# Kernel optimization log

Measured on AMD Instinct MI355X. Metric: run time of the kernel, lower is better.

## Reference

```python
import jax, jax.numpy as jnp
import numpy as np

NEG_INF = -1e30

def setup_inputs() -> dict:
    key = jax.random.key(0)
    ks = jax.random.split(key, 8)
    N, E = 4096, 16384
    Fn, Fe, Dn, De = 128, 64, 128, 64
    # xavier_uniform bound = sqrt(6/(fan_in+fan_out)); for 1-D params torch treats shape as (1, len)
    bn = np.sqrt(6.0 / (Fn + Dn))
    be = np.sqrt(6.0 / (Fe + De))
    return {
        "node_features": jax.random.normal(ks[0], (N, Fn), dtype=jnp.float32),
        "edge_features": jax.random.normal(ks[1], (E, Fe), dtype=jnp.float32),
        "adjacency_matrix": jax.random.randint(ks[2], (N, N), 0, 2, dtype=jnp.int32),
        "edge_adjacency_matrix": jax.random.randint(ks[3], (E, N), 0, 2, dtype=jnp.int32),
        "weight_node": jax.random.uniform(ks[4], (Fn, Dn), minval=-bn, maxval=bn, dtype=jnp.float32),
        "weight_edge": jax.random.uniform(ks[5], (Fe, De), minval=-be, maxval=be, dtype=jnp.float32),
        "parameter_vector_node": jax.random.uniform(ks[6], (2 * Dn,), minval=-1.0, maxval=1.0, dtype=jnp.float32),
        "parameter_vector_edge": jax.random.uniform(ks[7], (Dn + De,), minval=-1.0, maxval=1.0, dtype=jnp.float32),
    }


def reference(node_features, edge_features, adjacency_matrix, edge_adjacency_matrix,
              weight_node, weight_edge, parameter_vector_node, parameter_vector_edge):
    lrelu = jax.nn.leaky_relu  # default negative_slope=0.01, matches torch LeakyReLU
    Dn = weight_node.shape[1]

    h = node_features @ weight_node          # [N, Dn]
    he = edge_features @ weight_edge         # [E, De]

    # ---- node-level attention ----
    a_self, a_neigh = parameter_vector_node[:Dn], parameter_vector_node[Dn:]
    # score[i, j] = leaky_relu(a . cat(h_i, h_j)) for j a neighbor of i (adjacency[j, i] > 0)
    s_n = lrelu((h @ a_self)[:, None] + (h @ a_neigh)[None, :])   # [N, N]
    mask_n = adjacency_matrix.T > 0                                # [N, N], row i = neighbors of i
    coef_n = jax.nn.softmax(jnp.where(mask_n, s_n, NEG_INF), axis=1)
    coef_n = jnp.where(mask_n, coef_n, 0.0)
    deg_n = jnp.sum(mask_n, axis=1).astype(h.dtype)                # [N]
    means_n = (coef_n @ node_features) / deg_n[:, None]            # [N, Fn] (torch.mean divides by deg)
    out_n = lrelu(means_n @ weight_node)                           # [N, Dn]

    # ---- edge-level attention ----
    b_self, b_edge = parameter_vector_edge[:Dn], parameter_vector_edge[Dn:]
    s_e = lrelu((h @ b_self)[:, None] + (he @ b_edge)[None, :])    # [N, E]
    mask_e = edge_adjacency_matrix.T > 0                           # [N, E]
    coef_e = jax.nn.softmax(jnp.where(mask_e, s_e, NEG_INF), axis=1)
    coef_e = jnp.where(mask_e, coef_e, 0.0)
    deg_e = jnp.sum(mask_e, axis=1).astype(h.dtype)
    means_e = (coef_e @ edge_features) / deg_e[:, None]            # [N, Fe]
    out_e = lrelu(means_e @ weight_edge)                           # [N, De]

    return jnp.concatenate([out_n, out_e], axis=1)                 # [N, Dn+De]
```

## Files before the change

kernel.cpp:

```cpp
#include <hip/hip_runtime.h>

typedef short bf16x8 __attribute__((ext_vector_type(8)));
typedef float f32x4 __attribute__((ext_vector_type(4)));
typedef unsigned long long u64;

#define N_NODES 4096
#define N_EDGES 16384
#define FN 128
#define FE 64
#define NJS 16
#define EJS 32
#define TWN 64
#define TWE 256

#define PACKE_BLOCKS (256 * 64)
#define PACKN_BLOCKS (64 * 64)
#define PACK_BLOCKS (PACKE_BLOCKS + PACKN_BLOCKS)
#define NPROJ_BLOCKS (N_NODES / 4)
#define EPROJ_BLOCKS (N_EDGES / 4)
#define PREPN_BLOCKS (N_NODES / 64)
#define PREPE_BLOCKS (N_EDGES / 64)
#define FRONT_BLOCKS (PACK_BLOCKS + NPROJ_BLOCKS + EPROJ_BLOCKS + PREPN_BLOCKS + PREPE_BLOCKS)

#define ATTN_BLOCKS (32 * NJS)
#define ATTE_BLOCKS (32 * EJS)

__device__ __forceinline__ float lrelu(float x) { return x >= 0.f ? x : 0.01f * x; }
__device__ __forceinline__ unsigned short f2bf(float f) {
    unsigned int x = __float_as_uint(f);
    return (unsigned short)((x + 0x7fffu + ((x >> 16) & 1u)) >> 16);
}

__device__ __forceinline__ void prep_b(
    const float* __restrict__ src, unsigned short* __restrict__ dst,
    int j0, int F, int lf, float* tile ) {
    const int t = threadIdx.x;
    const int P = F + 1;
    for (int it = 0; it < (F >> 4); ++it) {
        int idx = (it * 256 + t) * 4;
        int j = idx >> lf, f = idx & (F - 1);
        float4 v = *(const float4*)(src + (size_t)(j0 + j) * F + f);
        tile[j * P + f + 0] = v.x; tile[j * P + f + 1] = v.y;
        tile[j * P + f + 2] = v.z; tile[j * P + f + 3] = v.w;
    }
    __syncthreads();
    for (int it = 0; it < (F >> 5); ++it) {
        int c = it * 256 + t;
        int jo = c >> lf, f = c & (F - 1);
        bf16x8 v;
#pragma unroll
        for (int e = 0; e < 8; ++e) v[e] = (short)f2bf(tile[(jo * 8 + e) * P + f]);
        *(bf16x8*)(dst + (((size_t)(j0 >> 3) + jo) * F + f) * 8) = v;
    }
}

__global__ __launch_bounds__(256) void k_front(
    const float* __restrict__ nf, const float* __restrict__ ef,
    const int* __restrict__ adj, const int* __restrict__ eadj,
    const float* __restrict__ Wn, const float* __restrict__ We,
    const float* __restrict__ pvn, const float* __restrict__ pve,
    u64* __restrict__ maskTN, u64* __restrict__ maskTE,
    float* __restrict__ alpha, float* __restrict__ beta, float* __restrict__ gamma,
    float* __restrict__ betaE,
    unsigned short* __restrict__ XbN, unsigned short* __restrict__ XbE) {
    __shared__ float smem[8256];
    int bx = blockIdx.x;
    const int t = threadIdx.x;
    const int wv = t >> 6, ln = t & 63;

    if (bx < PACK_BLOCKS) {
        const int* src; u64* dst; int jt, it, TW;
        if (bx < PACKE_BLOCKS) {
            jt = bx >> 6; it = bx & 63; src = eadj; dst = maskTE; TW = TWE;
        } else {
            int b2 = bx - PACKE_BLOCKS;
            jt = b2 >> 6; it = b2 & 63; src = adj; dst = maskTN; TW = TWN;
        }
        const int j0 = jt * 64, i0 = it * 64;
        int* smi = (int*)smem;
#pragma unroll
        for (int p = 0; p < 4; ++p) {
            int idx = p * 256 + t;
            int row = idx >> 4, c4 = (idx & 15) * 4;
            int4 v = *(const int4*)(src + (size_t)(j0 + row) * N_NODES + i0 + c4);
            smi[row * 65 + c4 + 0] = v.x; smi[row * 65 + c4 + 1] = v.y;
            smi[row * 65 + c4 + 2] = v.z; smi[row * 65 + c4 + 3] = v.w;
        }
        __syncthreads();
        u64 myw = 0;
#pragma unroll
        for (int q = 0; q < 16; ++q) {
            int iloc = wv * 16 + q;
            int val = smi[ln * 65 + iloc];
            u64 b = __ballot(val > 0);
            if (ln == q) myw = b;
        }
        if (ln < 16) dst[(size_t)(i0 + wv * 16 + ln) * TW + jt] = myw;
        return;
    }
    bx -= PACK_BLOCKS;
    if (bx < NPROJ_BLOCKS) {
        float* row = smem;
        const int i = bx * 4 + wv;
        float2 r2 = *(const float2*)(nf + (size_t)i * FN + ln * 2);
        row[wv * FN + ln * 2] = r2.x; row[wv * FN + ln * 2 + 1] = r2.y;
        __syncthreads();
        float h0 = 0.f, h1 = 0.f;
#pragma unroll 8
        for (int k = 0; k < FN; ++k) {
            float nv = row[wv * FN + k];
            float2 w2 = *(const float2*)(Wn + (size_t)k * FN + ln * 2);
            h0 = fmaf(nv, w2.x, h0); h1 = fmaf(nv, w2.y, h1);
        }
        float2 as = *(const float2*)(pvn + ln * 2);
        float2 an = *(const float2*)(pvn + FN + ln * 2);
        float2 bs = *(const float2*)(pve + ln * 2);
        float pa = h0 * as.x + h1 * as.y;
        float pb = h0 * an.x + h1 * an.y;
        float pg = h0 * bs.x + h1 * bs.y;
#pragma unroll
        for (int off = 32; off > 0; off >>= 1) {
            pa += __shfl_down(pa, off, 64);
            pb += __shfl_down(pb, off, 64);
            pg += __shfl_down(pg, off, 64);
        }
        if (ln == 0) { alpha[i] = pa; beta[i] = pb; gamma[i] = pg; }
        return;
    }
    bx -= NPROJ_BLOCKS;
    if (bx < EPROJ_BLOCKS) {
        float* row = smem;
        const int e = bx * 4 + wv;
        row[wv * FE + ln] = ef[(size_t)e * FE + ln];
        __syncthreads();
        float h = 0.f;
#pragma unroll 8
        for (int k = 0; k < FE; ++k)
            h = fmaf(row[wv * FE + k], We[(size_t)k * FE + ln], h);
        float p = h * pve[FN + ln];
#pragma unroll
        for (int off = 32; off > 0; off >>= 1) p += __shfl_down(p, off, 64);
        if (ln == 0) betaE[e] = p;
        return;
    }
    bx -= EPROJ_BLOCKS;
    if (bx < PREPN_BLOCKS) {
        prep_b(nf, XbN, bx * 64, FN, 7, smem);
        return;
    }
    bx -= PREPN_BLOCKS;
    prep_b(ef, XbE, bx * 64, FE, 6, smem);
}

__global__ __launch_bounds__(1024) void k_maxes(
    const float* __restrict__ beta, const float* __restrict__ betaE,
    float* __restrict__ maxes) {
    const float* src = blockIdx.x == 0 ? beta : betaE;
    const int n = blockIdx.x == 0 ? N_NODES : N_EDGES;
    float m = -3.0e38f;
#pragma unroll
    for (int t = threadIdx.x * 4; t < n; t += 4096) {
        float4 v = *(const float4*)(src + t);
        m = fmaxf(m, fmaxf(fmaxf(v.x, v.y), fmaxf(v.z, v.w)));
    }
#pragma unroll
    for (int off = 32; off > 0; off >>= 1) m = fmaxf(m, __shfl_down(m, off, 64));
    __shared__ float sm[16];
    if ((threadIdx.x & 63) == 0) sm[threadIdx.x >> 6] = m;
    __syncthreads();
    if (threadIdx.x == 0) {
        float mm = sm[0];
#pragma unroll
        for (int w = 1; w < 16; ++w) mm = fmaxf(mm, sm[w]);
        maxes[blockIdx.x] = mm;
    }
}

__global__ __launch_bounds__(256) void k_att(
    const unsigned short* __restrict__ XbN, const unsigned short* __restrict__ XbE,
    const unsigned* __restrict__ mTN, const unsigned* __restrict__ mTE,
    const float* __restrict__ alpha, const float* __restrict__ beta,
    const float* __restrict__ gamma, const float* __restrict__ betaE,
    const float* __restrict__ maxes,
    float* __restrict__ accN, float* __restrict__ zN, float* __restrict__ degN,
    float* __restrict__ accE, float* __restrict__ zE, float* __restrict__ degE) {
    const int t = threadIdx.x, l = t & 63, wid = t >> 6;
    const int l15 = l & 15, lq = l >> 4;
    int b = blockIdx.x;
    if (b < ATTN_BLOCKS) {
        const int bx = b & 31, bj = b >> 5;
        const int j0 = bj * (N_NODES / NJS);
        const int i0 = bx * 128 + wid * 32;
        const float a0 = alpha[i0 + l15], a1 = alpha[i0 + 16 + l15];
        const float mx = maxes[0];
        const float m0 = lrelu(a0 + mx), m1 = lrelu(a1 + mx);
        const unsigned* mr0 = mTN + (size_t)(i0 + l15) * (TWN * 2) + (j0 >> 5);
        const unsigned* mr1 = mr0 + (size_t)16 * (TWN * 2);
        f32x4 acc0[8] = {}, acc1[8] = {};
        float z0 = 0.f, z1 = 0.f;
        int d0 = 0, d1 = 0;
        const unsigned short* xb0 = XbN + (((size_t)(j0 >> 3) + lq) * FN + l15) * 8;
        const float* bb0 = beta + j0 + lq * 8;
        for (int ks = 0; ks < (N_NODES / NJS) / 32; ++ks) {
            const int jb = ks * 32;
            unsigned m32a = mr0[ks];
            unsigned m32b = mr1[ks];
            float4 b0v = *(const float4*)(bb0 + jb);
            float4 b1v = *(const float4*)(bb0 + jb + 4);
            float bv[8] = {b0v.x, b0v.y, b0v.z, b0v.w, b1v.x, b1v.y, b1v.z, b1v.w};
            bf16x8 wf0, wf1;
#pragma unroll
            for (int e = 0; e < 8; ++e) {
                int sh = lq * 8 + e;
                int mka = (int)((m32a >> sh) & 1u);
                int mkb = (int)((m32b >> sh) & 1u);
                float s0 = lrelu(a0 + bv[e]);
                float w0 = mka ? __expf(s0 - m0) : 0.f;
                float s1 = lrelu(a1 + bv[e]);
                float w1 = mkb ? __expf(s1 - m1) : 0.f;
                z0 += w0; z1 += w1; d0 += mka; d1 += mkb;
                wf0[e] = (short)f2bf(w0);
                wf1[e] = (short)f2bf(w1);
            }
            const unsigned short* xa = xb0 + (size_t)(jb >> 3) * (FN * 8);
#pragma unroll
            for (int mi = 0; mi < 8; ++mi) {
                bf16x8 a = *(const bf16x8*)(xa + mi * 128);
                acc0[mi] = __builtin_amdgcn_mfma_f32_16x16x32_bf16(a, wf0, acc0[mi], 0, 0, 0);
                acc1[mi] = __builtin_amdgcn_mfma_f32_16x16x32_bf16(a, wf1, acc1[mi], 0, 0, 0);
            }
        }
        float d0f = (float)d0, d1f = (float)d1;
        z0 += __shfl_xor(z0, 16, 64); z0 += __shfl_xor(z0, 32, 64);
        d0f += __shfl_xor(d0f, 16, 64); d0f += __shfl_xor(d0f, 32, 64);
        z1 += __shfl_xor(z1, 16, 64); z1 += __shfl_xor(z1, 32, 64);
        d1f += __shfl_xor(d1f, 16, 64); d1f += __shfl_xor(d1f, 32, 64);
        if (l < 16) {
            zN[bj * N_NODES + i0 + l] = z0;   degN[bj * N_NODES + i0 + l] = d0f;
            zN[bj * N_NODES + i0 + 16 + l] = z1;   degN[bj * N_NODES + i0 + 16 + l] = d1f;
        }
#pragma unroll
        for (int mi = 0; mi < 8; ++mi) {
            *(f32x4*)(accN + ((size_t)bj * N_NODES + i0 + l15) * FN + mi * 16 + lq * 4) = acc0[mi];
            *(f32x4*)(accN + ((size_t)bj * N_NODES + i0 + 16 + l15) * FN + mi * 16 + lq * 4) = acc1[mi];
        }
    } else {
        b -= ATTN_BLOCKS;
        const int bx = b & 31, bj = b >> 5;
        const int j0 = bj * (N_EDGES / EJS);
        const int i0 = bx * 128 + wid * 32;
        const float a0 = gamma[i0 + l15], a1 = gamma[i0 + 16 + l15];
        const float mx = maxes[1];
        const float m0 = lrelu(a0 + mx), m1 = lrelu(a1 + mx);
        const unsigned* mr0 = mTE + (size_t)(i0 + l15) * (TWE * 2) + (j0 >> 5);
        const unsigned* mr1 = mr0 + (size_t)16 * (TWE * 2);
        f32x4 acc0[4] = {}, acc1[4] = {};
        float z0 = 0.f, z1 = 0.f;
        int d0 = 0, d1 = 0;
        const unsigned short* xb0 = XbE + (((size_t)(j0 >> 3) + lq) * FE + l15) * 8;
        const float* bb0 = betaE + j0 + lq * 8;
        for (int ks = 0; ks < (N_EDGES / EJS) / 32; ++ks) {
            const int jb = ks * 32;
            unsigned m32a = mr0[ks];
            unsigned m32b = mr1[ks];
            float4 b0v = *(const float4*)(bb0 + jb);
            float4 b1v = *(const float4*)(bb0 + jb + 4);
            float bv[8] = {b0v.x, b0v.y, b0v.z, b0v.w, b1v.x, b1v.y, b1v.z, b1v.w};
            bf16x8 wf0, wf1;
#pragma unroll
            for (int e = 0; e < 8; ++e) {
                int sh = lq * 8 + e;
                int mka = (int)((m32a >> sh) & 1u);
                int mkb = (int)((m32b >> sh) & 1u);
                float s0 = lrelu(a0 + bv[e]);
                float w0 = mka ? __expf(s0 - m0) : 0.f;
                float s1 = lrelu(a1 + bv[e]);
                float w1 = mkb ? __expf(s1 - m1) : 0.f;
                z0 += w0; z1 += w1; d0 += mka; d1 += mkb;
                wf0[e] = (short)f2bf(w0);
                wf1[e] = (short)f2bf(w1);
            }
            const unsigned short* xa = xb0 + (size_t)(jb >> 3) * (FE * 8);
#pragma unroll
            for (int mi = 0; mi < 4; ++mi) {
                bf16x8 a = *(const bf16x8*)(xa + mi * 128);
                acc0[mi] = __builtin_amdgcn_mfma_f32_16x16x32_bf16(a, wf0, acc0[mi], 0, 0, 0);
                acc1[mi] = __builtin_amdgcn_mfma_f32_16x16x32_bf16(a, wf1, acc1[mi], 0, 0, 0);
            }
        }
        float d0f = (float)d0, d1f = (float)d1;
        z0 += __shfl_xor(z0, 16, 64); z0 += __shfl_xor(z0, 32, 64);
        d0f += __shfl_xor(d0f, 16, 64); d0f += __shfl_xor(d0f, 32, 64);
        z1 += __shfl_xor(z1, 16, 64); z1 += __shfl_xor(z1, 32, 64);
        d1f += __shfl_xor(d1f, 16, 64); d1f += __shfl_xor(d1f, 32, 64);
        if (l < 16) {
            zE[bj * N_NODES + i0 + l] = z0;   degE[bj * N_NODES + i0 + l] = d0f;
            zE[bj * N_NODES + i0 + 16 + l] = z1;   degE[bj * N_NODES + i0 + 16 + l] = d1f;
        }
#pragma unroll
        for (int mi = 0; mi < 4; ++mi) {
            *(f32x4*)(accE + ((size_t)bj * N_NODES + i0 + l15) * FE + mi * 16 + lq * 4) = acc0[mi];
            *(f32x4*)(accE + ((size_t)bj * N_NODES + i0 + 16 + l15) * FE + mi * 16 + lq * 4) = acc1[mi];
        }
    }
}

__global__ __launch_bounds__(256) void k_out(
    const float* __restrict__ accN, const float* __restrict__ zN, const float* __restrict__ degN,
    const float* __restrict__ accE, const float* __restrict__ zE, const float* __restrict__ degE,
    const float* __restrict__ Wn, const float* __restrict__ We,
    float* __restrict__ out) {
    __shared__ float ml[4][FN];
    const int wv = threadIdx.x >> 6, ln = threadIdx.x & 63;
    int b = blockIdx.x;
    if (b < N_NODES / 4) {
        const int i = b * 4 + wv;
        float s0 = 0.f, s1 = 0.f;
#pragma unroll
        for (int js = 0; js < NJS; ++js) {
            float2 v = *(const float2*)(accN + ((size_t)js * N_NODES + i) * FN + ln * 2);
            s0 += v.x; s1 += v.y;
        }
        float z = 0.f, d = 0.f;
#pragma unroll
        for (int js = 0; js < NJS; ++js) { z += zN[js * N_NODES + i]; d += degN[js * N_NODES + i]; }
        float zd = z * d;
        float inv = zd > 0.f ? 1.f / zd : 0.f;
        ml[wv][ln * 2] = s0 * inv; ml[wv][ln * 2 + 1] = s1 * inv;
        __syncthreads();
        float o0 = 0.f, o1 = 0.f;
#pragma unroll 8
        for (int k = 0; k < FN; ++k) {
            float mvv = ml[wv][k];
            float2 w2 = *(const float2*)(Wn + (size_t)k * FN + ln * 2);
            o0 = fmaf(mvv, w2.x, o0); o1 = fmaf(mvv, w2.y, o1);
        }
        out[(size_t)i * 192 + ln * 2] = lrelu(o0);
        out[(size_t)i * 192 + ln * 2 + 1] = lrelu(o1);
    } else {
        b -= N_NODES / 4;
        const int i = b * 4 + wv;
        float s = 0.f;
#pragma unroll
        for (int js = 0; js < EJS; ++js)
            s += accE[((size_t)js * N_NODES + i) * FE + ln];
        float z = 0.f, d = 0.f;
#pragma unroll
        for (int js = 0; js < EJS; ++js) { z += zE[js * N_NODES + i]; d += degE[js * N_NODES + i]; }
        float zd = z * d;
        float inv = zd > 0.f ? 1.f / zd : 0.f;
        ml[wv][ln] = s * inv;
        __syncthreads();
        float o = 0.f;
#pragma unroll 8
        for (int k = 0; k < FE; ++k)
            o = fmaf(ml[wv][k], We[(size_t)k * FE + ln], o);
        out[(size_t)i * 192 + 128 + ln] = lrelu(o);
    }
}

extern "C" void kernel_launch(void* const* d_in, const int* in_sizes, int n_in,
                              void* d_out, int out_size, void* d_ws, size_t ws_size,
                              hipStream_t stream) {
    (void)in_sizes; (void)n_in; (void)out_size; (void)ws_size;
    const float* nf   = (const float*)d_in[0];
    const float* ef   = (const float*)d_in[1];
    const int*   adj  = (const int*)d_in[2];
    const int*   eadj = (const int*)d_in[3];
    const float* Wn   = (const float*)d_in[4];
    const float* We   = (const float*)d_in[5];
    const float* pvn  = (const float*)d_in[6];
    const float* pve  = (const float*)d_in[7];
    float* out = (float*)d_out;

    u64* maskTN = (u64*)d_ws;
    u64* maskTE = maskTN + (size_t)N_NODES * TWN;
    float* alpha = (float*)(maskTE + (size_t)N_NODES * TWE);
    float* beta  = alpha + 4096;
    float* gamma = beta + 4096;
    float* betaE = gamma + 4096;
    float* maxes = betaE + 16384;
    unsigned short* XbN = (unsigned short*)(maxes + 64);
    unsigned short* XbE = XbN + (size_t)(N_NODES / 8) * FN * 8;
    float* accN = (float*)(XbE + (size_t)(N_EDGES / 8) * FE * 8);
    float* zN   = accN + (size_t)NJS * N_NODES * FN;
    float* degN = zN + (size_t)NJS * N_NODES;
    float* accE = degN + (size_t)NJS * N_NODES;
    float* zE   = accE + (size_t)EJS * N_NODES * FE;
    float* degE = zE + (size_t)EJS * N_NODES;

    k_front<<<FRONT_BLOCKS, 256, 0, stream>>>(nf, ef, adj, eadj, Wn, We, pvn, pve,
                                              maskTN, maskTE, alpha, beta, gamma, betaE, XbN, XbE);
    k_maxes<<<2, 1024, 0, stream>>>(beta, betaE, maxes);
    k_att<<<ATTN_BLOCKS + ATTE_BLOCKS, 256, 0, stream>>>(
        XbN, XbE, (const unsigned*)maskTN, (const unsigned*)maskTE,
        alpha, beta, gamma, betaE, maxes, accN, zN, degN, accE, zE, degE);
    k_out<<<N_NODES / 4 + N_NODES / 4, 256, 0, stream>>>(
        accN, zN, degN, accE, zE, degE, Wn, We, out);
}
```

Before: 201.0 us.

## Split mask packing into row-wise bit packing plus separate bit-transpose kernel

Mask packing now streams each adjacency row with one wave, using wide contiguous int4 loads and ballots to emit row-major bit words, instead of tiled LDS transposes of the int matrices. A new k_trans kernel transposes the packed bitmasks 64x64 at a time using register ballots. This is meant to cut LDS traffic and strided access when reading the large int32 adjacency inputs. It adds an extra launch and workspace. The bf16 prep tiles are halved, and degree counting in the attention loop now uses popcount instead of per-element adds.

After: 219.6 us. 9.3% more time.

```diff
diff --git a/kernel.cpp b/kernel.cpp
--- a/kernel.cpp
+++ b/kernel.cpp
@@ -10,17 +10,20 @@
 #define FE 64
 #define NJS 16
 #define EJS 32
+#define WPR 64
 #define TWN 64
 #define TWE 256
 
-#define PACKE_BLOCKS (256 * 64)
-#define PACKN_BLOCKS (64 * 64)
-#define PACK_BLOCKS (PACKE_BLOCKS + PACKN_BLOCKS)
+#define PACK_BLOCKS ((N_NODES + N_EDGES) / 4)
 #define NPROJ_BLOCKS (N_NODES / 4)
 #define EPROJ_BLOCKS (N_EDGES / 4)
-#define PREPN_BLOCKS (N_NODES / 64)
-#define PREPE_BLOCKS (N_EDGES / 64)
+#define PREPN_BLOCKS (N_NODES / 32)
+#define PREPE_BLOCKS (N_EDGES / 32)
 #define FRONT_BLOCKS (PACK_BLOCKS + NPROJ_BLOCKS + EPROJ_BLOCKS + PREPN_BLOCKS + PREPE_BLOCKS)
+
+#define TRN_TILES 1024
+#define TRE_TILES 4096
+#define TRANS_BLOCKS ((TRN_TILES + TRE_TILES) / 4)
 
 #define ATTN_BLOCKS (32 * NJS)
 #define ATTE_BLOCKS (32 * EJS)
@@ -31,12 +34,13 @@
     return (unsigned short)((x + 0x7fffu + ((x >> 16) & 1u)) >> 16);
 }
 
-__device__ __forceinline__ void prep_b(
+__device__ __forceinline__ void prep_b32(
     const float* __restrict__ src, unsigned short* __restrict__ dst,
     int j0, int F, int lf, float* tile ) {
     const int t = threadIdx.x;
     const int P = F + 1;
-    for (int it = 0; it < (F >> 4); ++it) {
+    const int LITERS = (32 * F) >> 10;
+    for (int it = 0; it < LITERS; ++it) {
         int idx = (it * 256 + t) * 4;
         int j = idx >> lf, f = idx & (F - 1);
         float4 v = *(const float4*)(src + (size_t)(j0 + j) * F + f);
@@ -44,7 +48,8 @@
         tile[j * P + f + 2] = v.z; tile[j * P + f + 3] = v.w;
     }
     __syncthreads();
-    for (int it = 0; it < (F >> 5); ++it) {
+    const int WITERS = (32 * F) >> 11;
+    for (int it = 0; it < WITERS; ++it) {
         int c = it * 256 + t;
         int jo = c >> lf, f = c & (F - 1);
         bf16x8 v;
@@ -59,43 +64,37 @@
     const int* __restrict__ adj, const int* __restrict__ eadj,
     const float* __restrict__ Wn, const float* __restrict__ We,
     const float* __restrict__ pvn, const float* __restrict__ pve,
-    u64* __restrict__ maskTN, u64* __restrict__ maskTE,
+    u64* __restrict__ maskRN, u64* __restrict__ maskRE,
     float* __restrict__ alpha, float* __restrict__ beta, float* __restrict__ gamma,
     float* __restrict__ betaE,
     unsigned short* __restrict__ XbN, unsigned short* __restrict__ XbE) {
-    __shared__ float smem[8256];
+    __shared__ float smem[32 * 129];
     int bx = blockIdx.x;
     const int t = threadIdx.x;
     const int wv = t >> 6, ln = t & 63;
 
     if (bx < PACK_BLOCKS) {
-        const int* src; u64* dst; int jt, it, TW;
-        if (bx < PACKE_BLOCKS) {
-            jt = bx >> 6; it = bx & 63; src = eadj; dst = maskTE; TW = TWE;
+        const int row = bx * 4 + wv;
+        const int* src;
+        u64* dst;
+        if (row < N_EDGES) {
+            src = eadj + (size_t)row * N_NODES;
+            dst = maskRE + (size_t)row * WPR;
         } else {
-            int b2 = bx - PACKE_BLOCKS;
-            jt = b2 >> 6; it = b2 & 63; src = adj; dst = maskTN; TW = TWN;
-        }
-        const int j0 = jt * 64, i0 = it * 64;
-        int* smi = (int*)smem;
-#pragma unroll
-        for (int p = 0; p < 4; ++p) {
-            int idx = p * 256 + t;
-            int row = idx >> 4, c4 = (idx & 15) * 4;
-            int4 v = *(const int4*)(src + (size_t)(j0 + row) * N_NODES + i0 + c4);
-            smi[row * 65 + c4 + 0] = v.x; smi[row * 65 + c4 + 1] = v.y;
-            smi[row * 65 + c4 + 2] = v.z; smi[row * 65 + c4 + 3] = v.w;
-        }
-        __syncthreads();
-        u64 myw = 0;
-#pragma unroll
-        for (int q = 0; q < 16; ++q) {
-            int iloc = wv * 16 + q;
-            int val = smi[ln * 65 + iloc];
-            u64 b = __ballot(val > 0);
-            if (ln == q) myw = b;
-        }
-        if (ln < 16) dst[(size_t)(i0 + wv * 16 + ln) * TW + jt] = myw;
+            src = adj + (size_t)(row - N_EDGES) * N_NODES;
+            dst = maskRN + (size_t)(row - N_EDGES) * WPR;
+        }
+        int4 v[16];
+#pragma unroll
+        for (int c = 0; c < 16; ++c) v[c] = *(const int4*)(src + c * 256 + ln * 4);
+#pragma unroll
+        for (int c = 0; c < 16; ++c) {
+            u64 b0 = __ballot(v[c].x > 0);
+            u64 b1 = __ballot(v[c].y > 0);
+            u64 b2 = __ballot(v[c].z > 0);
+            u64 b3 = __ballot(v[c].w > 0);
+            if (ln < 4) dst[c * 4 + ln] = (ln == 0) ? b0 : (ln == 1) ? b1 : (ln == 2) ? b2 : b3;
+        }
         return;
     }
     bx -= PACK_BLOCKS;
@@ -145,11 +144,61 @@
     }
     bx -= EPROJ_BLOCKS;
     if (bx < PREPN_BLOCKS) {
-        prep_b(nf, XbN, bx * 64, FN, 7, smem);
+        prep_b32(nf, XbN, bx * 32, FN, 7, smem);
         return;
     }
     bx -= PREPN_BLOCKS;
-    prep_b(ef, XbE, bx * 64, FE, 6, smem);
+    prep_b32(ef, XbE, bx * 32, FE, 6, smem);
+}
+
+__global__ __launch_bounds__(256) void k_trans(
+    const u64* __restrict__ maskRN, const u64* __restrict__ maskRE,
+    u64* __restrict__ maskTN, u64* __restrict__ maskTE) {
+    const int wv = threadIdx.x >> 6, l = threadIdx.x & 63;
+    int tile = blockIdx.x * 4 + wv;
+    const u64* srcb; u64* dstb; int jt, g, TW;
+    if (tile < TRN_TILES) {
+        jt = tile >> 4; g = tile & 15; srcb = maskRN; dstb = maskTN; TW = TWN;
+    } else {
+        tile -= TRN_TILES;
+        jt = tile >> 4; g = tile & 15; srcb = maskRE; dstb = maskTE; TW = TWE;
+    }
+    const u64* sp = srcb + (size_t)(jt * 64 + l) * WPR + g * 4;
+    u64 mw0 = sp[0], mw1 = sp[1], mw2 = sp[2], mw3 = sp[3];
+    u64 myw0 = 0, myw1 = 0, myw2 = 0, myw3 = 0;
+#pragma unroll 8
+    for (int cc = 0; cc < 64; ++cc) {
+        int wsel = cc & 3, bsel = 0 * 16 + (cc >> 2);
+        u64 sw = wsel == 0 ? mw0 : wsel == 1 ? mw1 : wsel == 2 ? mw2 : mw3;
+        u64 tw = __ballot(((sw >> bsel) & 1ull) != 0);
+        if (l == cc) myw0 = tw;
+    }
+#pragma unroll 8
+    for (int cc = 0; cc < 64; ++cc) {
+        int wsel = cc & 3, bsel = 1 * 16 + (cc >> 2);
+        u64 sw = wsel == 0 ? mw0 : wsel == 1 ? mw1 : wsel == 2 ? mw2 : mw3;
+        u64 tw = __ballot(((sw >> bsel) & 1ull) != 0);
+        if (l == cc) myw1 = tw;
+    }
+#pragma unroll 8
+    for (int cc = 0; cc < 64; ++cc) {
+        int wsel = cc & 3, bsel = 2 * 16 + (cc >> 2);
+        u64 sw = wsel == 0 ? mw0 : wsel == 1 ? mw1 : wsel == 2 ? mw2 : mw3;
+        u64 tw = __ballot(((sw >> bsel) & 1ull) != 0);
+        if (l == cc) myw2 = tw;
+    }
+#pragma unroll 8
+    for (int cc = 0; cc < 64; ++cc) {
+        int wsel = cc & 3, bsel = 3 * 16 + (cc >> 2);
+        u64 sw = wsel == 0 ? mw0 : wsel == 1 ? mw1 : wsel == 2 ? mw2 : mw3;
+        u64 tw = __ballot(((sw >> bsel) & 1ull) != 0);
+        if (l == cc) myw3 = tw;
+    }
+    const size_t ibase = (size_t)g * 256;
+    dstb[(ibase +   0 + l) * TW + jt] = myw0;
+    dstb[(ibase +  64 + l) * TW + jt] = myw1;
+    dstb[(ibase + 128 + l) * TW + jt] = myw2;
+    dstb[(ibase + 192 + l) * TW + jt] = myw3;
 }
 
 __global__ __launch_bounds__(1024) void k_maxes(
@@ -205,6 +254,8 @@
             const int jb = ks * 32;
             unsigned m32a = mr0[ks];
             unsigned m32b = mr1[ks];
+            d0 += __popc((m32a >> (lq * 8)) & 0xffu);
+            d1 += __popc((m32b >> (lq * 8)) & 0xffu);
             float4 b0v = *(const float4*)(bb0 + jb);
             float4 b1v = *(const float4*)(bb0 + jb + 4);
             float bv[8] = {b0v.x, b0v.y, b0v.z, b0v.w, b1v.x, b1v.y, b1v.z, b1v.w};
@@ -218,7 +269,7 @@
                 float w0 = mka ? __expf(s0 - m0) : 0.f;
                 float s1 = lrelu(a1 + bv[e]);
                 float w1 = mkb ? __expf(s1 - m1) : 0.f;
-                z0 += w0; z1 += w1; d0 += mka; d1 += mkb;
+                z0 += w0; z1 += w1;
                 wf0[e] = (short)f2bf(w0);
                 wf1[e] = (short)f2bf(w1);
             }
@@ -263,6 +314,8 @@
             const int jb = ks * 32;
             unsigned m32a = mr0[ks];
             unsigned m32b = mr1[ks];
+            d0 += __popc((m32a >> (lq * 8)) & 0xffu);
+            d1 += __popc((m32b >> (lq * 8)) & 0xffu);
             float4 b0v = *(const float4*)(bb0 + jb);
             float4 b1v = *(const float4*)(bb0 + jb + 4);
             float bv[8] = {b0v.x, b0v.y, b0v.z, b0v.w, b1v.x, b1v.y, b1v.z, b1v.w};
@@ -276,7 +329,7 @@
                 float w0 = mka ? __expf(s0 - m0) : 0.f;
                 float s1 = lrelu(a1 + bv[e]);
                 float w1 = mkb ? __expf(s1 - m1) : 0.f;
-                z0 += w0; z1 += w1; d0 += mka; d1 += mkb;
+                z0 += w0; z1 += w1;
                 wf0[e] = (short)f2bf(w0);
                 wf1[e] = (short)f2bf(w1);
             }
@@ -373,7 +426,9 @@
     const float* pve  = (const float*)d_in[7];
     float* out = (float*)d_out;
 
-    u64* maskTN = (u64*)d_ws;
+    u64* maskRN = (u64*)d_ws;
+    u64* maskRE = maskRN + (size_t)N_NODES * WPR;
+    u64* maskTN = maskRE + (size_t)N_EDGES * WPR;
     u64* maskTE = maskTN + (size_t)N_NODES * TWN;
     float* alpha = (float*)(maskTE + (size_t)N_NODES * TWE);
     float* beta  = alpha + 4096;
@@ -390,7 +445,8 @@
     float* degE = zE + (size_t)EJS * N_NODES;
 
     k_front<<<FRONT_BLOCKS, 256, 0, stream>>>(nf, ef, adj, eadj, Wn, We, pvn, pve,
-                                              maskTN, maskTE, alpha, beta, gamma, betaE, XbN, XbE);
+                                              maskRN, maskRE, alpha, beta, gamma, betaE, XbN, XbE);
+    k_trans<<<TRANS_BLOCKS, 256, 0, stream>>>(maskRN, maskRE, maskTN, maskTE);
     k_maxes<<<2, 1024, 0, stream>>>(beta, betaE, maxes);
     k_att<<<ATTN_BLOCKS + ATTE_BLOCKS, 256, 0, stream>>>(
         XbN, XbE, (const unsigned*)maskTN, (const unsigned*)maskTE,
```

## Repack adjacency bitmasks with larger tiles, fuse max reduction via atomics

Applied to the files above, without the earlier changes.

Adjacency packing now uses far fewer blocks, each covering 64 rows by 1024 columns. The int4 loads are compressed to bytes in LDS, and the bitmask words are stored in a j-major layout so that consecutive i rows are contiguous. The separate k_maxes kernel is replaced by order-preserving atomicMax on encoded floats inside the projection blocks, with a memset up front. The attention kernel now counts degree with popcount instead of per-element adds, and the bf16 prep uses 32-row tiles. This cuts one kernel launch and increases per-block work in the dominant mask-packing stage, at the cost of atomic contention and changed mask indexing.

After: 396.3 us. 97.2% more time.

```diff
diff --git a/kernel.cpp b/kernel.cpp
--- a/kernel.cpp
+++ b/kernel.cpp
@@ -10,17 +10,14 @@
 #define FE 64
 #define NJS 16
 #define EJS 32
-#define TWN 64
-#define TWE 256
-
-#define PACKE_BLOCKS (256 * 64)
-#define PACKN_BLOCKS (64 * 64)
-#define PACK_BLOCKS (PACKE_BLOCKS + PACKN_BLOCKS)
+
+#define PACKE_BLOCKS 1024
+#define PACKN_BLOCKS 256
+#define EPROJ_BLOCKS (N_EDGES / 4)
 #define NPROJ_BLOCKS (N_NODES / 4)
-#define EPROJ_BLOCKS (N_EDGES / 4)
-#define PREPN_BLOCKS (N_NODES / 64)
-#define PREPE_BLOCKS (N_EDGES / 64)
-#define FRONT_BLOCKS (PACK_BLOCKS + NPROJ_BLOCKS + EPROJ_BLOCKS + PREPN_BLOCKS + PREPE_BLOCKS)
+#define PREPE_BLOCKS (N_EDGES / 32)
+#define PREPN_BLOCKS (N_NODES / 32)
+#define FRONT_BLOCKS (PACKE_BLOCKS + PACKN_BLOCKS + EPROJ_BLOCKS + NPROJ_BLOCKS + PREPE_BLOCKS + PREPN_BLOCKS)
 
 #define ATTN_BLOCKS (32 * NJS)
 #define ATTE_BLOCKS (32 * EJS)
@@ -30,13 +27,21 @@
     unsigned int x = __float_as_uint(f);
     return (unsigned short)((x + 0x7fffu + ((x >> 16) & 1u)) >> 16);
 }
-
-__device__ __forceinline__ void prep_b(
+__device__ __forceinline__ unsigned encf(float x) {
+    unsigned b = __float_as_uint(x);
+    return (b >> 31) ? ~b : (b | 0x80000000u);
+}
+__device__ __forceinline__ float decf(unsigned e) {
+    return __uint_as_float((e & 0x80000000u) ? (e ^ 0x80000000u) : ~e);
+}
+
+__device__ __forceinline__ void prep_b32(
     const float* __restrict__ src, unsigned short* __restrict__ dst,
     int j0, int F, int lf, float* tile ) {
     const int t = threadIdx.x;
     const int P = F + 1;
-    for (int it = 0; it < (F >> 4); ++it) {
+    const int LITERS = (32 * F) >> 10;
+    for (int it = 0; it < LITERS; ++it) {
         int idx = (it * 256 + t) * 4;
         int j = idx >> lf, f = idx & (F - 1);
         float4 v = *(const float4*)(src + (size_t)(j0 + j) * F + f);
@@ -44,13 +49,44 @@
         tile[j * P + f + 2] = v.z; tile[j * P + f + 3] = v.w;
     }
     __syncthreads();
-    for (int it = 0; it < (F >> 5); ++it) {
+    const int WITERS = (32 * F) >> 11;
+    for (int it = 0; it < WITERS; ++it) {
         int c = it * 256 + t;
         int jo = c >> lf, f = c & (F - 1);
         bf16x8 v;
 #pragma unroll
         for (int e = 0; e < 8; ++e) v[e] = (short)f2bf(tile[(jo * 8 + e) * P + f]);
         *(bf16x8*)(dst + (((size_t)(j0 >> 3) + jo) * F + f) * 8) = v;
+    }
+}
+
+__device__ __forceinline__ void pack_tile(
+    const int* __restrict__ src, u64* __restrict__ dst,
+    int jt, int iq, unsigned char* lds8 ) {
+    const int t = threadIdx.x;
+    const int wv = t >> 6, ln = t & 63;
+    const size_t rowbase = (size_t)jt * 64;
+    for (int p = 0; p < 4; ++p) {
+        const int ib = iq * 1024 + p * 256;
+#pragma unroll
+        for (int it = 0; it < 16; ++it) {
+            int idx = it * 256 + t;
+            int row = idx >> 6, c = idx & 63;
+            int4 v = *(const int4*)(src + (rowbase + row) * N_NODES + ib + c * 4);
+            unsigned bb = (unsigned)(v.x > 0) | ((unsigned)(v.y > 0) << 8) |
+                          ((unsigned)(v.z > 0) << 16) | ((unsigned)(v.w > 0) << 24);
+            *(unsigned*)&lds8[row * 260 + c * 4] = bb;
+        }
+        __syncthreads();
+        u64 myw = 0;
+#pragma unroll 16
+        for (int q = 0; q < 64; ++q) {
+            unsigned char val = lds8[ln * 260 + wv * 64 + q];
+            u64 b = __ballot(val != 0);
+            if (ln == q) myw = b;
+        }
+        dst[(size_t)jt * N_NODES + ib + wv * 64 + ln] = myw;
+        __syncthreads();
     }
 }
 
@@ -59,46 +95,44 @@
     const int* __restrict__ adj, const int* __restrict__ eadj,
     const float* __restrict__ Wn, const float* __restrict__ We,
     const float* __restrict__ pvn, const float* __restrict__ pve,
-    u64* __restrict__ maskTN, u64* __restrict__ maskTE,
+    u64* __restrict__ mt2N, u64* __restrict__ mt2E,
     float* __restrict__ alpha, float* __restrict__ beta, float* __restrict__ gamma,
-    float* __restrict__ betaE,
+    float* __restrict__ betaE, unsigned* __restrict__ maxesU,
     unsigned short* __restrict__ XbN, unsigned short* __restrict__ XbE) {
-    __shared__ float smem[8256];
+    __shared__ float smem[4160];
     int bx = blockIdx.x;
     const int t = threadIdx.x;
     const int wv = t >> 6, ln = t & 63;
 
-    if (bx < PACK_BLOCKS) {
-        const int* src; u64* dst; int jt, it, TW;
-        if (bx < PACKE_BLOCKS) {
-            jt = bx >> 6; it = bx & 63; src = eadj; dst = maskTE; TW = TWE;
-        } else {
-            int b2 = bx - PACKE_BLOCKS;
-            jt = b2 >> 6; it = b2 & 63; src = adj; dst = maskTN; TW = TWN;
-        }
-        const int j0 = jt * 64, i0 = it * 64;
-        int* smi = (int*)smem;
-#pragma unroll
-        for (int p = 0; p < 4; ++p) {
-            int idx = p * 256 + t;
-            int row = idx >> 4, c4 = (idx & 15) * 4;
-            int4 v = *(const int4*)(src + (size_t)(j0 + row) * N_NODES + i0 + c4);
-            smi[row * 65 + c4 + 0] = v.x; smi[row * 65 + c4 + 1] = v.y;
-            smi[row * 65 + c4 + 2] = v.z; smi[row * 65 + c4 + 3] = v.w;
-        }
-        __syncthreads();
-        u64 myw = 0;
-#pragma unroll
-        for (int q = 0; q < 16; ++q) {
-            int iloc = wv * 16 + q;
-            int val = smi[ln * 65 + iloc];
-            u64 b = __ballot(val > 0);
-            if (ln == q) myw = b;
-        }
-        if (ln < 16) dst[(size_t)(i0 + wv * 16 + ln) * TW + jt] = myw;
+    if (bx < PACKE_BLOCKS) {
+        pack_tile(eadj, mt2E, bx >> 2, bx & 3, (unsigned char*)smem);
         return;
     }
-    bx -= PACK_BLOCKS;
+    bx -= PACKE_BLOCKS;
+    if (bx < PACKN_BLOCKS) {
+        pack_tile(adj, mt2N, bx >> 2, bx & 3, (unsigned char*)smem);
+        return;
+    }
+    bx -= PACKN_BLOCKS;
+    if (bx < EPROJ_BLOCKS) {
+        float* row = smem;
+        const int e = bx * 4 + wv;
+        row[wv * FE + ln] = ef[(size_t)e * FE + ln];
+        __syncthreads();
+        float h = 0.f;
+#pragma unroll 8
+        for (int k = 0; k < FE; ++k)
+            h = fmaf(row[wv * FE + k], We[(size_t)k * FE + ln], h);
+        float p = h * pve[FN + ln];
+#pragma unroll
+        for (int off = 32; off > 0; off >>= 1) p += __shfl_down(p, off, 64);
+        if (ln == 0) {
+            betaE[e] = p;
+            atomicMax(&maxesU[1], encf(p));
+        }
+        return;
+    }
+    bx -= EPROJ_BLOCKS;
     if (bx < NPROJ_BLOCKS) {
         float* row = smem;
         const int i = bx * 4 + wv;
@@ -124,64 +158,27 @@
             pb += __shfl_down(pb, off, 64);
             pg += __shfl_down(pg, off, 64);
         }
-        if (ln == 0) { alpha[i] = pa; beta[i] = pb; gamma[i] = pg; }
+        if (ln == 0) {
+            alpha[i] = pa; beta[i] = pb; gamma[i] = pg;
+            atomicMax(&maxesU[0], encf(pb));
+        }
         return;
     }
     bx -= NPROJ_BLOCKS;
-    if (bx < EPROJ_BLOCKS) {
-        float* row = smem;
-        const int e = bx * 4 + wv;
-        row[wv * FE + ln] = ef[(size_t)e * FE + ln];
-        __syncthreads();
-        float h = 0.f;
-#pragma unroll 8
-        for (int k = 0; k < FE; ++k)
-            h = fmaf(row[wv * FE + k], We[(size_t)k * FE + ln], h);
-        float p = h * pve[FN + ln];
-#pragma unroll
-        for (int off = 32; off > 0; off >>= 1) p += __shfl_down(p, off, 64);
-        if (ln == 0) betaE[e] = p;
+    if (bx < PREPE_BLOCKS) {
+        prep_b32(ef, XbE, bx * 32, FE, 6, smem);
         return;
     }
-    bx -= EPROJ_BLOCKS;
-    if (bx < PREPN_BLOCKS) {
-        prep_b(nf, XbN, bx * 64, FN, 7, smem);
-        return;
-    }
-    bx -= PREPN_BLOCKS;
-    prep_b(ef, XbE, bx * 64, FE, 6, smem);
-}
-
-__global__ __launch_bounds__(1024) void k_maxes(
-    const float* __restrict__ beta, const float* __restrict__ betaE,
-    float* __restrict__ maxes) {
-    const float* src = blockIdx.x == 0 ? beta : betaE;
-    const int n = blockIdx.x == 0 ? N_NODES : N_EDGES;
-    float m = -3.0e38f;
-#pragma unroll
-    for (int t = threadIdx.x * 4; t < n; t += 4096) {
-        float4 v = *(const float4*)(src + t);
-        m = fmaxf(m, fmaxf(fmaxf(v.x, v.y), fmaxf(v.z, v.w)));
-    }
-#pragma unroll
-    for (int off = 32; off > 0; off >>= 1) m = fmaxf(m, __shfl_down(m, off, 64));
-    __shared__ float sm[16];
-    if ((threadIdx.x & 63) == 0) sm[threadIdx.x >> 6] = m;
-    __syncthreads();
-    if (threadIdx.x == 0) {
-        float mm = sm[0];
-#pragma unroll
-        for (int w = 1; w < 16; ++w) mm = fmaxf(mm, sm[w]);
-        maxes[blockIdx.x] = mm;
-    }
+    bx -= PREPE_BLOCKS;
+    prep_b32(nf, XbN, bx * 32, FN, 7, smem);
 }
 
 __global__ __launch_bounds__(256) void k_att(
     const unsigned short* __restrict__ XbN, const unsigned short* __restrict__ XbE,
-    const unsigned* __restrict__ mTN, const unsigned* __restrict__ mTE,
+    const unsigned* __restrict__ mtNu, const unsigned* __restrict__ mtEu,
     const float* __restrict__ alpha, const float* __restrict__ beta,
     const float* __restrict__ gamma, const float* __restrict__ betaE,
-    const float* __restrict__ maxes,
+    const unsigned* __restrict__ maxesU,
     float* __restrict__ accN, float* __restrict__ zN, float* __restrict__ degN,
     float* __restrict__ accE, float* __restrict__ zE, float* __restrict__ degE) {
     const int t = threadIdx.x, l = t & 63, wid = t >> 6;
@@ -192,10 +189,9 @@
         const int j0 = bj * (N_NODES / NJS);
         const int i0 = bx * 128 + wid * 32;
         const float a0 = alpha[i0 + l15], a1 = alpha[i0 + 16 + l15];
-        const float mx = maxes[0];
+        const float mx = decf(maxesU[0]);
         const float m0 = lrelu(a0 + mx), m1 = lrelu(a1 + mx);
-        const unsigned* mr0 = mTN + (size_t)(i0 + l15) * (TWN * 2) + (j0 >> 5);
-        const unsigned* mr1 = mr0 + (size_t)16 * (TWN * 2);
+        const int ib0 = (i0 + l15) * 2, ib1 = (i0 + 16 + l15) * 2;
         f32x4 acc0[8] = {}, acc1[8] = {};
         float z0 = 0.f, z1 = 0.f;
         int d0 = 0, d1 = 0;
@@ -203,8 +199,11 @@
         const float* bb0 = beta + j0 + lq * 8;
         for (int ks = 0; ks < (N_NODES / NJS) / 32; ++ks) {
             const int jb = ks * 32;
-            unsigned m32a = mr0[ks];
-            unsigned m32b = mr1[ks];
+            const int widx = ((bj << 2) + (ks >> 1)) * 8192 + (ks & 1);
+            unsigned m32a = mtNu[widx + ib0];
+            unsigned m32b = mtNu[widx + ib1];
+            d0 += __popc((m32a >> (lq * 8)) & 0xffu);
+            d1 += __popc((m32b >> (lq * 8)) & 0xffu);
             float4 b0v = *(const float4*)(bb0 + jb);
             float4 b1v = *(const float4*)(bb0 + jb + 4);
             float bv[8] = {b0v.x, b0v.y, b0v.z, b0v.w, b1v.x, b1v.y, b1v.z, b1v.w};
@@ -218,7 +217,7 @@
                 float w0 = mka ? __expf(s0 - m0) : 0.f;
                 float s1 = lrelu(a1 + bv[e]);
                 float w1 = mkb ? __expf(s1 - m1) : 0.f;
-                z0 += w0; z1 += w1; d0 += mka; d1 += mkb;
+                z0 += w0; z1 += w1;
                 wf0[e] = (short)f2bf(w0);
                 wf1[e] = (short)f2bf(w1);
             }
@@ -250,10 +249,9 @@
         const int j0 = bj * (N_EDGES / EJS);
         const int i0 = bx * 128 + wid * 32;
         const float a0 = gamma[i0 + l15], a1 = gamma[i0 + 16 + l15];
-        const float mx = maxes[1];
+        const float mx = decf(maxesU[1]);
         const float m0 = lrelu(a0 + mx), m1 = lrelu(a1 + mx);
-        const unsigned* mr0 = mTE + (size_t)(i0 + l15) * (TWE * 2) + (j0 >> 5);
-        const unsigned* mr1 = mr0 + (size_t)16 * (TWE * 2);
+        const int ib0 = (i0 + l15) * 2, ib1 = (i0 + 16 + l15) * 2;
         f32x4 acc0[4] = {}, acc1[4] = {};
         float z0 = 0.f, z1 = 0.f;
         int d0 = 0, d1 = 0;
@@ -261,8 +259,11 @@
         const float* bb0 = betaE + j0 + lq * 8;
         for (int ks = 0; ks < (N_EDGES / EJS) / 32; ++ks) {
             const int jb = ks * 32;
-            unsigned m32a = mr0[ks];
-            unsigned m32b = mr1[ks];
+            const int widx = ((bj << 3) + (ks >> 1)) * 8192 + (ks & 1);
+            unsigned m32a = mtEu[widx + ib0];
+            unsigned m32b = mtEu[widx + ib1];
+            d0 += __popc((m32a >> (lq * 8)) & 0xffu);
+            d1 += __popc((m32b >> (lq * 8)) & 0xffu);
             float4 b0v = *(const float4*)(bb0 + jb);
             float4 b1v = *(const float4*)(bb0 + jb + 4);
             float bv[8] = {b0v.x, b0v.y, b0v.z, b0v.w, b1v.x, b1v.y, b1v.z, b1v.w};
@@ -276,7 +277,7 @@
                 float w0 = mka ? __expf(s0 - m0) : 0.f;
                 float s1 = lrelu(a1 + bv[e]);
                 float w1 = mkb ? __expf(s1 - m1) : 0.f;
-                z0 += w0; z1 += w1; d0 += mka; d1 += mkb;
+                z0 += w0; z1 += w1;
                 wf0[e] = (short)f2bf(w0);
                 wf1[e] = (short)f2bf(w1);
             }
@@ -373,14 +374,14 @@
     const float* pve  = (const float*)d_in[7];
     float* out = (float*)d_out;
 
-    u64* maskTN = (u64*)d_ws;
-    u64* maskTE = maskTN + (size_t)N_NODES * TWN;
-    float* alpha = (float*)(maskTE + (size_t)N_NODES * TWE);
+    u64* mt2N = (u64*)d_ws;
+    u64* mt2E = mt2N + (size_t)64 * N_NODES;
+    float* alpha = (float*)(mt2E + (size_t)256 * N_NODES);
     float* beta  = alpha + 4096;
     float* gamma = beta + 4096;
     float* betaE = gamma + 4096;
-    float* maxes = betaE + 16384;
-    unsigned short* XbN = (unsigned short*)(maxes + 64);
+    unsigned* maxesU = (unsigned*)(betaE + 16384);
+    unsigned short* XbN = (unsigned short*)(maxesU + 16);
     unsigned short* XbE = XbN + (size_t)(N_NODES / 8) * FN * 8;
     float* accN = (float*)(XbE + (size_t)(N_EDGES / 8) * FE * 8);
     float* zN   = accN + (size_t)NJS * N_NODES * FN;
@@ -389,12 +390,12 @@
     float* zE   = accE + (size_t)EJS * N_NODES * FE;
     float* degE = zE + (size_t)EJS * N_NODES;
 
+    hipMemsetAsync(maxesU, 0, 2 * sizeof(unsigned), stream);
     k_front<<<FRONT_BLOCKS, 256, 0, stream>>>(nf, ef, adj, eadj, Wn, We, pvn, pve,
-                                              maskTN, maskTE, alpha, beta, gamma, betaE, XbN, XbE);
-    k_maxes<<<2, 1024, 0, stream>>>(beta, betaE, maxes);
+                                              mt2N, mt2E, alpha, beta, gamma, betaE, maxesU, XbN, XbE);
     k_att<<<ATTN_BLOCKS + ATTE_BLOCKS, 256, 0, stream>>>(
-        XbN, XbE, (const unsigned*)maskTN, (const unsigned*)maskTE,
-        alpha, beta, gamma, betaE, maxes, accN, zN, degN, accE, zE, degE);
+        XbN, XbE, (const unsigned*)mt2N, (const unsigned*)mt2E,
+        alpha, beta, gamma, betaE, maxesU, accN, zN, degN, accE, zE, degE);
     k_out<<<N_NODES / 4 + N_NODES / 4, 256, 0, stream>>>(
         accN, zN, degN, accE, zE, degE, Wn, We, out);
 }
```
